# Kernel tuning notes

Measured on AMD Instinct MI355X. Metric: run time of the kernel, lower is better.

The kernel has to match this reference:

```python
import jax, jax.numpy as jnp
import numpy as np

B, N, D = 4, 4096, 1024
H, HD = 16, 64            # num_heads, head_dim (dim // num_heads)
K_ANCHOR = 256
SCALE = 1.0 / np.sqrt(float(HD))


def setup_inputs() -> dict:
    key = jax.random.key(0)
    ks = jax.random.split(key, 12)
    init = lambda k, shape, fan_in: jax.random.normal(k, shape, jnp.float32) * (1.0 / np.sqrt(fan_in))
    return {
        "x": jax.random.normal(ks[0], (B, N, D), jnp.float32),
        "Wq": init(ks[1], (D, H * HD), D), "bq": jnp.zeros((H * HD,), jnp.float32),
        "Wk": init(ks[2], (D, H * HD), D), "bk": jnp.zeros((H * HD,), jnp.float32),
        "Wv": init(ks[3], (D, H * HD), D), "bv": jnp.zeros((H * HD,), jnp.float32),
        "Wqt": init(ks[4], (D, D), D),     "bqt": jnp.zeros((D,), jnp.float32),
        "Wo": init(ks[5], (H * HD, D), H * HD), "bo": jnp.zeros((D,), jnp.float32),
        "num_anchor_tokens": K_ANCHOR,
    }


def _split_heads(t):
    # [B, S, H*HD] -> [B, H, S, HD]
    b, s, _ = t.shape
    return t.reshape(b, s, H, HD).transpose(0, 2, 1, 3)


def reference(x, Wq, bq, Wk, bk, Wv, bv, Wqt, bqt, Wo, bo, num_anchor_tokens):
    K = num_anchor_tokens  # static python int
    anchors = x[:, :K]     # [B, K, D]
    queries = x[:, K:]     # [B, N-K, D]

    q_a = anchors @ Wq + bq           # [B, K, H*HD]
    k_a = anchors @ Wk + bk           # [B, K, H*HD]
    v_a = anchors @ Wv + bv           # [B, K, H*HD]
    q_q = queries @ Wqt + bqt         # [B, N-K, H*HD] (dim == H*HD)

    q = _split_heads(jnp.concatenate([q_a, q_q], axis=1))  # [B, H, N, HD]
    k = _split_heads(k_a)                                  # [B, H, K, HD]
    v = _split_heads(v_a)                                  # [B, H, K, HD]

    scores = jnp.einsum("bhnd,bhkd->bhnk", q, k) * SCALE   # [B, H, N, K]
    weights = jax.nn.softmax(scores, axis=-1)
    ctx = jnp.einsum("bhnk,bhkd->bhnd", weights, v)        # [B, H, N, HD]
    ctx = ctx.transpose(0, 2, 1, 3).reshape(x.shape[0], x.shape[1], H * HD)
    return ctx @ Wo + bo               # [B, N, D]
```

## Files before the change

kernel.cpp:

```cpp
#include <hip/hip_runtime.h>
#include <stdint.h>
#include <stddef.h>


typedef _Float16 v8hf __attribute__((ext_vector_type(8)));
typedef _Float16 h4   __attribute__((ext_vector_type(4)));
typedef float    f32x4 __attribute__((ext_vector_type(4)));

#define ATT_SCALE 0.125f
#define LOG2E     1.44269504088896340736f

__device__ __forceinline__ void async16(const void* g, void* l) {
  __builtin_amdgcn_global_load_lds(
      (const __attribute__((address_space(1))) void*)g,
      (__attribute__((address_space(3))) void*)l,
      16, 0, 0);
}

__global__ __launch_bounds__(256) void cvt_kernel(const float* __restrict__ src,
                                                  _Float16* __restrict__ dst, int n) {
  int i = (blockIdx.x * 256 + threadIdx.x) * 4;
  if (i + 3 < n) {
    float4 v = *(const float4*)(src + i);
    h4 o; o[0] = (_Float16)v.x; o[1] = (_Float16)v.y; o[2] = (_Float16)v.z; o[3] = (_Float16)v.w;
    *(h4*)(dst + i) = o;
  }
}

struct TPArgs { const float* src[5]; _Float16* dst[5]; };

__global__ __launch_bounds__(256) void transpose5_k(TPArgs a) {
  __shared__ _Float16 t[32][33];
  const int z = blockIdx.z;
  const float* __restrict__ src = a.src[z];
  _Float16* __restrict__ dst = a.dst[z];
  const int bx = blockIdx.x * 32, by = blockIdx.y * 32;
  const int x = threadIdx.x;
  for (int yy = threadIdx.y; yy < 32; yy += 8)
    t[yy][x] = (_Float16)src[(size_t)(by + yy) * 1024 + bx + x];
  __syncthreads();
  for (int yy = threadIdx.y; yy < 32; yy += 8)
    dst[(size_t)(bx + yy) * 1024 + by + x] = t[x][yy];
}

template <typename OutT>
__global__ __launch_bounds__(512, 2) void gemm256(
    const _Float16* __restrict__ A, const _Float16* __restrict__ Bt,
    const float* __restrict__ bias, OutT* __restrict__ out,
    int rowsPerBatch, int rowStart)
{
  __shared__ __attribute__((aligned(16))) _Float16 As[4 * 256 * 32];
  __shared__ __attribute__((aligned(16))) _Float16 Bs[4 * 256 * 32];

  const int tid  = threadIdx.x;
  const int wave = tid >> 6, lane = tid & 63;
  const int quad = lane >> 4, l16 = lane & 15;
  const int wr = wave >> 2, wc = wave & 3;

  const int nwg = gridDim.x * gridDim.y;
  const int lin = blockIdx.y * 4 + blockIdx.x;
  const int swz = (lin & 7) * (nwg >> 3) + (lin >> 3);
  const int bx = swz & 3, by = swz >> 2;

  const int lrow = lane >> 2, lblk = lane & 3;

  auto gRowOf = [&](int m) -> int {
    int b = m / rowsPerBatch;
    return b * 4096 + rowStart + (m - b * rowsPerBatch);
  };

  const int tr0 = wave * 16 + lrow;
  const int tr1 = 128 + tr0;
  const _Float16* aS0 = A  + (size_t)gRowOf(by * 256 + tr0) * 1024 + (lblk ^ ((tr0 >> 1) & 3)) * 8;
  const _Float16* aS1 = A  + (size_t)gRowOf(by * 256 + tr1) * 1024 + (lblk ^ ((tr1 >> 1) & 3)) * 8;
  const _Float16* bS0 = Bt + (size_t)(bx * 256 + tr0) * 1024 + (lblk ^ ((tr0 >> 1) & 3)) * 8;
  const _Float16* bS1 = Bt + (size_t)(bx * 256 + tr1) * 1024 + (lblk ^ ((tr1 >> 1) & 3)) * 8;

  auto stage = [&](int t) {
    const int k0 = t * 32;
    _Float16* ad = As + (t & 3) * 8192 + wave * 512;
    _Float16* bd = Bs + (t & 3) * 8192 + wave * 512;
    async16(aS0 + k0, ad);
    async16(aS1 + k0, ad + 4096);
    async16(bS0 + k0, bd);
    async16(bS1 + k0, bd + 4096);
  };

  const int fblk = (quad ^ ((l16 >> 1) & 3)) * 8;

  f32x4 acc[8][4];
  #pragma unroll
  for (int i = 0; i < 8; i++)
    #pragma unroll
    for (int j = 0; j < 4; j++)
      acc[i][j] = f32x4{0.f, 0.f, 0.f, 0.f};

  stage(0); stage(1); stage(2);

  #pragma unroll 1
  for (int t = 0; t < 32; ++t) {
    if (t < 30)       asm volatile("s_waitcnt vmcnt(8)" ::: "memory");
    else if (t == 30) asm volatile("s_waitcnt vmcnt(4)" ::: "memory");
    else              asm volatile("s_waitcnt vmcnt(0)" ::: "memory");
    __builtin_amdgcn_s_barrier();
    __builtin_amdgcn_sched_barrier(0);
    asm volatile("" ::: "memory");

    if (t + 3 < 32) stage(t + 3);

    const _Float16* Ab = As + (t & 3) * 8192;
    const _Float16* Bb = Bs + (t & 3) * 8192;
    v8hf af[8], bf[4];
    #pragma unroll
    for (int nt = 0; nt < 4; nt++)
      bf[nt] = *(const v8hf*)(Bb + (wc * 64 + nt * 16 + l16) * 32 + fblk);
    #pragma unroll
    for (int mt = 0; mt < 8; mt++)
      af[mt] = *(const v8hf*)(Ab + (wr * 128 + mt * 16 + l16) * 32 + fblk);

    __builtin_amdgcn_s_setprio(1);
    #pragma unroll
    for (int mt = 0; mt < 8; mt++)
      #pragma unroll
      for (int nt = 0; nt < 4; nt++)
        acc[mt][nt] = __builtin_amdgcn_mfma_f32_16x16x32_f16(af[mt], bf[nt], acc[mt][nt], 0, 0, 0);
    __builtin_amdgcn_s_setprio(0);
  }

  const int colBase = bx * 256 + wc * 64;
  const int rowBase = by * 256 + wr * 128;
  #pragma unroll
  for (int mt = 0; mt < 8; mt++) {
    #pragma unroll
    for (int r = 0; r < 4; r++) {
      int m = rowBase + mt * 16 + quad * 4 + r;
      int b = m / rowsPerBatch;
      int rr = m - b * rowsPerBatch;
      #pragma unroll
      for (int nt = 0; nt < 4; nt++) {
        int col = colBase + nt * 16 + l16;
        float v = acc[mt][nt][r] + bias[col];
        out[(size_t)(b * 4096 + rowStart + rr) * 1024 + col] = (OutT)v;
      }
    }
  }
}

template <typename OutT>
__global__ __launch_bounds__(256) void gemm64(
    const _Float16* __restrict__ A, const _Float16* __restrict__ Bt,
    const float* __restrict__ bias0, const float* __restrict__ bias1,
    const float* __restrict__ bias2,
    OutT* __restrict__ out0, _Float16* __restrict__ out1, _Float16* __restrict__ out2,
    int rowsPerBatch, int rowStart, int mode)
{
  __shared__ __attribute__((aligned(16))) _Float16 As[64 * 32];
  __shared__ __attribute__((aligned(16))) _Float16 Bs[128 * 32];

  const int tid  = threadIdx.x;
  const int wave = tid >> 6, lane = tid & 63;
  const int quad = lane >> 4, l16 = lane & 15;
  const int wr = wave >> 1, wc = wave & 1;

  const int gx = gridDim.x;
  const int lin = blockIdx.y * gx + blockIdx.x;
  const int x8 = lin & 7, j = lin >> 3;
  const int bx = j % gx;
  const int by = x8 * (gridDim.y >> 3) + j / gx;

  const int srow = lane >> 2;
  const int skol = (((lane & 3) ^ ((lane >> 3) & 3)) * 8);

  auto gRowOf = [&](int m) -> int {
    int b = m / rowsPerBatch;
    int r = m - b * rowsPerBatch;
    return b * 4096 + rowStart + r;
  };

  const int bc0 = wave * 2, bc1 = bc0 + 1;
  const _Float16* aS  = A  + (size_t)gRowOf(by * 64 + wave * 16 + srow) * 1024 + skol;
  const _Float16* bS0 = Bt + (size_t)(bx * 128 + bc0 * 16 + srow) * 1024 + skol;
  const _Float16* bS1 = Bt + (size_t)(bx * 128 + bc1 * 16 + srow) * 1024 + skol;
  _Float16* aD  = As + wave * 512;
  _Float16* bD0 = Bs + bc0 * 512;
  _Float16* bD1 = Bs + bc1 * 512;

  const int fblk = (quad ^ ((l16 >> 1) & 3)) * 8;

  f32x4 acc[2][4];
  #pragma unroll
  for (int i = 0; i < 2; i++)
    #pragma unroll
    for (int jj = 0; jj < 4; jj++)
      acc[i][jj] = f32x4{0.f, 0.f, 0.f, 0.f};

  for (int k0 = 0; k0 < 1024; k0 += 32) {
    __syncthreads();
    async16(aS  + k0, aD);
    async16(bS0 + k0, bD0);
    async16(bS1 + k0, bD1);
    __syncthreads();

    v8hf af[2], bfr[4];
    #pragma unroll
    for (int mt = 0; mt < 2; mt++)
      af[mt] = *(const v8hf*)(As + (wr * 32 + mt * 16 + l16) * 32 + fblk);
    #pragma unroll
    for (int nt = 0; nt < 4; nt++)
      bfr[nt] = *(const v8hf*)(Bs + (wc * 64 + nt * 16 + l16) * 32 + fblk);
    #pragma unroll
    for (int mt = 0; mt < 2; mt++)
      #pragma unroll
      for (int nt = 0; nt < 4; nt++)
        acc[mt][nt] = __builtin_amdgcn_mfma_f32_16x16x32_f16(af[mt], bfr[nt], acc[mt][nt], 0, 0, 0);
  }

  const int colBase = bx * 128 + wc * 64;
  const int rowBase = by * 64 + wr * 32;
  #pragma unroll
  for (int mt = 0; mt < 2; mt++) {
    #pragma unroll
    for (int r = 0; r < 4; r++) {
      int m = rowBase + mt * 16 + quad * 4 + r;
      int b = m / rowsPerBatch;
      int rr = m - b * rowsPerBatch;
      #pragma unroll
      for (int nt = 0; nt < 4; nt++) {
        int col = colBase + nt * 16 + l16;
        float v = acc[mt][nt][r];
        if (mode == 0) {
          v += bias0[col];
          out0[(size_t)(b * 4096 + rowStart + rr) * 1024 + col] = (OutT)v;
        } else {
          if (col < 1024) {
            v += bias0[col];
            out0[(size_t)(b * 4096 + rr) * 1024 + col] = (OutT)v;
          } else if (col < 2048) {
            int c2 = col - 1024;
            v += bias1[c2];
            out1[(size_t)(b * 256 + rr) * 1024 + c2] = (_Float16)v;
          } else {
            int c2 = col - 2048;
            v += bias2[c2];
            out2[(size_t)((b * 16 + (c2 >> 6)) * 64 + (c2 & 63)) * 256 + rr] = (_Float16)v;
          }
        }
      }
    }
  }
}

__global__ __launch_bounds__(256) void attn_kernel(
    const _Float16* __restrict__ q, const _Float16* __restrict__ k,
    const _Float16* __restrict__ vt, _Float16* __restrict__ ctx)
{
  __shared__ __attribute__((aligned(16))) _Float16 KP[256 * 64];
  __shared__ __attribute__((aligned(16))) _Float16 Vs[64 * 256];

  const int tid  = threadIdx.x;
  const int wave = tid >> 6, lane = tid & 63;
  const int quad = lane >> 4, l16 = lane & 15;
  const int bid = blockIdx.x;
  const int qt = bid & 63, h = (bid >> 6) & 15, b = bid >> 10;

  const int fq = (l16 ^ (l16 >> 1)) & 7;

  const _Float16* kbase = k + (size_t)b * 256 * 1024 + h * 64;
  {
    const int s = lane >> 3;
    const int p = lane & 7;
    #pragma unroll
    for (int i = 0; i < 8; i++) {
      int c = wave * 8 + i;
      int row = c * 8 + s;
      int f = (row ^ (row >> 1)) & 7;
      int dblk = p ^ f;
      async16(kbase + (size_t)row * 1024 + dblk * 8, KP + c * 512);
    }
  }

  const int qrow = qt * 64 + wave * 16 + l16;
  const _Float16* qbase = q + (size_t)(b * 4096 + qrow) * 1024 + h * 64 + quad * 8;
  v8hf a0 = *(const v8hf*)(qbase);
  v8hf a1 = *(const v8hf*)(qbase + 32);

  f32x4 s[16];
  #pragma unroll
  for (int t = 0; t < 16; t++) s[t] = f32x4{0.f, 0.f, 0.f, 0.f};

  __syncthreads();

  #pragma unroll
  for (int t = 0; t < 16; t++) {
    const _Float16* rbase = KP + (t * 16 + l16) * 64;
    int pb0 = (quad ^ fq) * 8;
    v8hf b0 = *(const v8hf*)(rbase + pb0);
    v8hf b1 = *(const v8hf*)(rbase + (pb0 ^ 32));
    s[t] = __builtin_amdgcn_mfma_f32_16x16x32_f16(a0, b0, s[t], 0, 0, 0);
    s[t] = __builtin_amdgcn_mfma_f32_16x16x32_f16(a1, b1, s[t], 0, 0, 0);
  }

  const float ce = ATT_SCALE * LOG2E;
  float inv[4];
  #pragma unroll
  for (int r = 0; r < 4; r++) {
    float m = s[0][r];
    #pragma unroll
    for (int t = 1; t < 16; t++) m = fmaxf(m, s[t][r]);
    m = fmaxf(m, __shfl_xor(m, 1));
    m = fmaxf(m, __shfl_xor(m, 2));
    m = fmaxf(m, __shfl_xor(m, 4));
    m = fmaxf(m, __shfl_xor(m, 8));
    float sum = 0.f;
    #pragma unroll
    for (int t = 0; t < 16; t++) {
      float e = exp2f((s[t][r] - m) * ce);
      s[t][r] = e;
      sum += e;
    }
    sum += __shfl_xor(sum, 1);
    sum += __shfl_xor(sum, 2);
    sum += __shfl_xor(sum, 4);
    sum += __shfl_xor(sum, 8);
    inv[r] = 1.0f / sum;
  }

  __syncthreads();

  const _Float16* vbase = vt + (size_t)(b * 16 + h) * 16384;
  {
    const int p = lane & 31;
    #pragma unroll
    for (int i = 0; i < 8; i++) {
      int c = wave * 8 + i;
      int d = c * 2 + (lane >> 5);
      int f = (d ^ (d >> 1)) & 7;
      int kblk = p ^ f;
      async16(vbase + d * 256 + kblk * 8, Vs + c * 512);
    }
  }

  #pragma unroll
  for (int r = 0; r < 4; r++) {
    int qr = wave * 16 + quad * 4 + r;
    int fp = (qr ^ (qr >> 1)) & 7;
    _Float16* prow = KP + qr * 256;
    #pragma unroll
    for (int t = 0; t < 16; t++) {
      int key = t * 16 + l16;
      prow[(((key >> 3) ^ fp) * 8) + (key & 7)] = (_Float16)(s[t][r] * inv[r]);
    }
  }

  __syncthreads();

  f32x4 o[4];
  #pragma unroll
  for (int nt = 0; nt < 4; nt++) o[nt] = f32x4{0.f, 0.f, 0.f, 0.f};
  #pragma unroll
  for (int c = 0; c < 8; c++) {
    int kblk = c * 4 + quad;
    v8hf pa = *(const v8hf*)(KP + (wave * 16 + l16) * 256 + (kblk ^ fq) * 8);
    #pragma unroll
    for (int nt = 0; nt < 4; nt++) {
      v8hf vb = *(const v8hf*)(Vs + (nt * 16 + l16) * 256 + (kblk ^ fq) * 8);
      o[nt] = __builtin_amdgcn_mfma_f32_16x16x32_f16(pa, vb, o[nt], 0, 0, 0);
    }
  }

  _Float16* obase = ctx + (size_t)(b * 4096 + qt * 64 + wave * 16 + quad * 4) * 1024 + h * 64;
  #pragma unroll
  for (int nt = 0; nt < 4; nt++)
    #pragma unroll
    for (int r = 0; r < 4; r++)
      obase[(size_t)r * 1024 + nt * 16 + l16] = (_Float16)o[nt][r];
}

extern "C" void kernel_launch(void* const* d_in, const int* in_sizes, int n_in,
                              void* d_out, int out_size, void* d_ws, size_t ws_size,
                              hipStream_t stream)
{
  (void)in_sizes; (void)n_in; (void)out_size; (void)ws_size;

  const float* x   = (const float*)d_in[0];
  const float* Wq  = (const float*)d_in[1];
  const float* bq  = (const float*)d_in[2];
  const float* Wk  = (const float*)d_in[3];
  const float* bk  = (const float*)d_in[4];
  const float* Wv  = (const float*)d_in[5];
  const float* bv  = (const float*)d_in[6];
  const float* Wqt = (const float*)d_in[7];
  const float* bqt = (const float*)d_in[8];
  const float* Wo  = (const float*)d_in[9];
  const float* bo  = (const float*)d_in[10];

  char* ws = (char*)d_ws;
  _Float16* xh    = (_Float16*)(ws);
  _Float16* WtQKV = (_Float16*)(ws + (32ll << 20));
  _Float16* WtQT  = (_Float16*)(ws + (38ll << 20));
  _Float16* WtO   = (_Float16*)(ws + (40ll << 20));
  _Float16* qbuf  = (_Float16*)(ws + (42ll << 20));
  _Float16* kbuf  = (_Float16*)(ws + (74ll << 20));
  _Float16* vtb   = (_Float16*)(ws + (76ll << 20));
  _Float16* ctxb  = (_Float16*)(ws + (78ll << 20));
  float* outp = (float*)d_out;

  const int nx = 4 * 4096 * 1024;
  cvt_kernel<<<nx / 1024, 256, 0, stream>>>(x, xh, nx);

  TPArgs tpa;
  tpa.src[0] = Wq;  tpa.dst[0] = WtQKV;
  tpa.src[1] = Wk;  tpa.dst[1] = WtQKV + 1024 * 1024;
  tpa.src[2] = Wv;  tpa.dst[2] = WtQKV + 2 * 1024 * 1024;
  tpa.src[3] = Wqt; tpa.dst[3] = WtQT;
  tpa.src[4] = Wo;  tpa.dst[4] = WtO;
  transpose5_k<<<dim3(32, 32, 5), dim3(32, 8), 0, stream>>>(tpa);

  gemm64<_Float16><<<dim3(24, 16), 256, 0, stream>>>(xh, WtQKV, bq, bk, bv,
                                                     qbuf, kbuf, vtb, 256, 0, 1);
  gemm256<_Float16><<<dim3(4, 60), 512, 0, stream>>>(xh, WtQT, bqt,
                                                     qbuf, 3840, 256);
  attn_kernel<<<4096, 256, 0, stream>>>(qbuf, kbuf, vtb, ctxb);
  gemm256<float><<<dim3(4, 64), 512, 0, stream>>>(ctxb, WtO, bo,
                                                  outp, 4096, 0);
}
```

Measured before the change: 331.5 us.

## Fold softmax scale into Q projection, prefetch V early, pack P stores, defer normalization

```diff
diff --git a/kernel.cpp b/kernel.cpp
--- a/kernel.cpp
+++ b/kernel.cpp
@@ -6,15 +6,22 @@
 typedef _Float16 v8hf __attribute__((ext_vector_type(8)));
 typedef _Float16 h4   __attribute__((ext_vector_type(4)));
 typedef float    f32x4 __attribute__((ext_vector_type(4)));
+typedef uint32_t u32x4 __attribute__((ext_vector_type(4)));
 
 #define ATT_SCALE 0.125f
 #define LOG2E     1.44269504088896340736f
+#define QK_CE     (ATT_SCALE * LOG2E)
 
 __device__ __forceinline__ void async16(const void* g, void* l) {
   __builtin_amdgcn_global_load_lds(
       (const __attribute__((address_space(1))) void*)g,
       (__attribute__((address_space(3))) void*)l,
       16, 0, 0);
+}
+
+__device__ __forceinline__ uint32_t pk_h2(float a, float b) {
+  auto w = __builtin_amdgcn_cvt_pkrtz(a, b);
+  return __builtin_bit_cast(uint32_t, w);
 }
 
 __global__ __launch_bounds__(256) void cvt_kernel(const float* __restrict__ src,
@@ -47,7 +54,7 @@
 __global__ __launch_bounds__(512, 2) void gemm256(
     const _Float16* __restrict__ A, const _Float16* __restrict__ Bt,
     const float* __restrict__ bias, OutT* __restrict__ out,
-    int rowsPerBatch, int rowStart)
+    int rowsPerBatch, int rowStart, float oscale)
 {
   __shared__ __attribute__((aligned(16))) _Float16 As[4 * 256 * 32];
   __shared__ __attribute__((aligned(16))) _Float16 Bs[4 * 256 * 32];
@@ -139,7 +146,7 @@
       #pragma unroll
       for (int nt = 0; nt < 4; nt++) {
         int col = colBase + nt * 16 + l16;
-        float v = acc[mt][nt][r] + bias[col];
+        float v = (acc[mt][nt][r] + bias[col]) * oscale;
         out[(size_t)(b * 4096 + rowStart + rr) * 1024 + col] = (OutT)v;
       }
     }
@@ -233,7 +240,7 @@
           out0[(size_t)(b * 4096 + rowStart + rr) * 1024 + col] = (OutT)v;
         } else {
           if (col < 1024) {
-            v += bias0[col];
+            v = (v + bias0[col]) * QK_CE;
             out0[(size_t)(b * 4096 + rr) * 1024 + col] = (OutT)v;
           } else if (col < 2048) {
             int c2 = col - 1024;
@@ -242,7 +249,8 @@
           } else {
             int c2 = col - 2048;
             v += bias2[c2];
-            out2[(size_t)((b * 16 + (c2 >> 6)) * 64 + (c2 & 63)) * 256 + rr] = (_Float16)v;
+            int pr = ((rr & 15) << 4) | (rr >> 4);
+            out2[(size_t)((b * 16 + (c2 >> 6)) * 64 + (c2 & 63)) * 256 + pr] = (_Float16)v;
           }
         }
       }
@@ -274,8 +282,19 @@
       int c = wave * 8 + i;
       int row = c * 8 + s;
       int f = (row ^ (row >> 1)) & 7;
-      int dblk = p ^ f;
-      async16(kbase + (size_t)row * 1024 + dblk * 8, KP + c * 512);
+      async16(kbase + (size_t)row * 1024 + (p ^ f) * 8, KP + c * 512);
+    }
+  }
+
+  const _Float16* vbase = vt + (size_t)(b * 16 + h) * 16384;
+  {
+    const int p = lane & 31;
+    #pragma unroll
+    for (int i = 0; i < 8; i++) {
+      int c = wave * 8 + i;
+      int d = c * 2 + (lane >> 5);
+      int f = (d ^ (d >> 1)) & 7;
+      async16(vbase + d * 256 + (p ^ f) * 8, Vs + c * 512);
     }
   }
 
@@ -300,13 +319,15 @@
     s[t] = __builtin_amdgcn_mfma_f32_16x16x32_f16(a1, b1, s[t], 0, 0, 0);
   }
 
-  const float ce = ATT_SCALE * LOG2E;
   float inv[4];
   #pragma unroll
   for (int r = 0; r < 4; r++) {
-    float m = s[0][r];
-    #pragma unroll
-    for (int t = 1; t < 16; t++) m = fmaxf(m, s[t][r]);
+    float m01 = fmaxf(s[0][r], s[1][r]),   m23 = fmaxf(s[2][r], s[3][r]);
+    float m45 = fmaxf(s[4][r], s[5][r]),   m67 = fmaxf(s[6][r], s[7][r]);
+    float m89 = fmaxf(s[8][r], s[9][r]),   mab = fmaxf(s[10][r], s[11][r]);
+    float mcd = fmaxf(s[12][r], s[13][r]), mef = fmaxf(s[14][r], s[15][r]);
+    float m = fmaxf(fmaxf(fmaxf(m01, m23), fmaxf(m45, m67)),
+                    fmaxf(fmaxf(m89, mab), fmaxf(mcd, mef)));
     m = fmaxf(m, __shfl_xor(m, 1));
     m = fmaxf(m, __shfl_xor(m, 2));
     m = fmaxf(m, __shfl_xor(m, 4));
@@ -314,7 +335,7 @@
     float sum = 0.f;
     #pragma unroll
     for (int t = 0; t < 16; t++) {
-      float e = exp2f((s[t][r] - m) * ce);
+      float e = exp2f(s[t][r] - m);
       s[t][r] = e;
       sum += e;
     }
@@ -327,32 +348,23 @@
 
   __syncthreads();
 
-  const _Float16* vbase = vt + (size_t)(b * 16 + h) * 16384;
-  {
-    const int p = lane & 31;
-    #pragma unroll
-    for (int i = 0; i < 8; i++) {
-      int c = wave * 8 + i;
-      int d = c * 2 + (lane >> 5);
-      int f = (d ^ (d >> 1)) & 7;
-      int kblk = p ^ f;
-      async16(vbase + d * 256 + kblk * 8, Vs + c * 512);
-    }
-  }
-
   #pragma unroll
   for (int r = 0; r < 4; r++) {
-    int qr = wave * 16 + quad * 4 + r;
-    int fp = (qr ^ (qr >> 1)) & 7;
-    _Float16* prow = KP + qr * 256;
-    #pragma unroll
-    for (int t = 0; t < 16; t++) {
-      int key = t * 16 + l16;
-      prow[(((key >> 3) ^ fp) * 8) + (key & 7)] = (_Float16)(s[t][r] * inv[r]);
-    }
-  }
-
-  __syncthreads();
+    const int qr = quad * 4 + r;
+    const int fp = (qr ^ (qr >> 1)) & 7;
+    _Float16* prow = KP + (wave * 16 + qr) * 256;
+    u32x4 lo, hi;
+    #pragma unroll
+    for (int j = 0; j < 4; j++) {
+      lo[j] = pk_h2(s[2 * j][r],     s[2 * j + 1][r]);
+      hi[j] = pk_h2(s[2 * j + 8][r], s[2 * j + 9][r]);
+    }
+    *(u32x4*)(prow + ((2 * l16) ^ fp) * 8)     = lo;
+    *(u32x4*)(prow + ((2 * l16 + 1) ^ fp) * 8) = hi;
+  }
+
+  asm volatile("s_waitcnt lgkmcnt(0)" ::: "memory");
+  __builtin_amdgcn_sched_barrier(0);
 
   f32x4 o[4];
   #pragma unroll
@@ -373,7 +385,7 @@
   for (int nt = 0; nt < 4; nt++)
     #pragma unroll
     for (int r = 0; r < 4; r++)
-      obase[(size_t)r * 1024 + nt * 16 + l16] = (_Float16)o[nt][r];
+      obase[(size_t)r * 1024 + nt * 16 + l16] = (_Float16)(o[nt][r] * inv[r]);
 }
 
 extern "C" void kernel_launch(void* const* d_in, const int* in_sizes, int n_in,
@@ -419,8 +431,8 @@
   gemm64<_Float16><<<dim3(24, 16), 256, 0, stream>>>(xh, WtQKV, bq, bk, bv,
                                                      qbuf, kbuf, vtb, 256, 0, 1);
   gemm256<_Float16><<<dim3(4, 60), 512, 0, stream>>>(xh, WtQT, bqt,
-                                                     qbuf, 3840, 256);
+                                                     qbuf, 3840, 256, QK_CE);
   attn_kernel<<<4096, 256, 0, stream>>>(qbuf, kbuf, vtb, ctxb);
   gemm256<float><<<dim3(4, 64), 512, 0, stream>>>(ctxb, WtO, bo,
-                                                  outp, 4096, 0);
-}
+                                                  outp, 4096, 0, 1.0f);
+}
```

Measured after the change: 324.7 us. 2.0% less time.
